# Kernel tuning notes

Hardware: AMD Instinct MI355X
Metric: run time of the kernel (lower is better)

The kernel has to match this reference:

```python
import jax, jax.numpy as jnp
import numpy as np

B, F, K = 8192, 4096, 64


def setup_inputs() -> dict:
    key = jax.random.key(0)
    kx, kv = jax.random.split(key)
    x = jax.random.normal(kx, (B, F), dtype=jnp.float32)
    # original init: uniform(-0.01, 0.01)
    v = jax.random.uniform(kv, (F, K), dtype=jnp.float32, minval=-0.01, maxval=0.01)
    return {"x": x, "v": v}


def reference(x, v):
    # sum_{i<j} <v_i, v_j> x_i x_j  ==  0.5 * sum_f ((x@v)_f^2 - (x^2 @ v^2)_f)
    xv = x @ v                      # [B, K]
    x2v2 = (x * x) @ (v * v)        # [B, K]
    res = 0.5 * jnp.sum(xv * xv - x2v2, axis=-1, keepdims=True)  # [B, 1]
    return res
```

## Files before the change

kernel.cpp:

```cpp
#include <hip/hip_runtime.h>
#include <hip/hip_bf16.h>


#define F_DIM 4096
#define K_DIM 64
#define B_ROWS 8192

typedef __attribute__((ext_vector_type(8))) short short8;
typedef __attribute__((ext_vector_type(4))) float float4v;
typedef __attribute__((ext_vector_type(16))) float f32x16;

__device__ __forceinline__ short f2bs(float f) {
    __hip_bfloat16 h = __float2bfloat16(f);
    short s;
    __builtin_memcpy(&s, &h, 2);
    return s;
}

__global__ void prep_kernel(const float* __restrict__ v,
                            short* __restrict__ vtf,
                            float* __restrict__ w) {
    __shared__ short lds_t[4][64][16];

    const int wid  = threadIdx.x >> 6;
    const int lane = threadIdx.x & 63;
    const int fc   = blockIdx.x * 4 + wid;
    const int r    = lane >> 2;
    const int k0   = (lane & 3) * 16;

    const float* src = v + (size_t)(fc * 16 + r) * K_DIM + k0;
    float vals[16];
#pragma unroll
    for (int i = 0; i < 16; i += 4) {
        float4v t = *(const float4v*)(src + i);
        vals[i] = t.x; vals[i+1] = t.y; vals[i+2] = t.z; vals[i+3] = t.w;
    }

    float sq = 0.0f;
#pragma unroll
    for (int i = 0; i < 16; ++i) sq += vals[i] * vals[i];
    sq += __shfl_xor(sq, 1, 64);
    sq += __shfl_xor(sq, 2, 64);
    if ((lane & 3) == 0) w[fc * 16 + r] = sq;

#pragma unroll
    for (int kk = 0; kk < 16; ++kk) lds_t[wid][k0 + kk][r] = f2bs(vals[kk]);
    __syncthreads();

#pragma unroll
    for (int c = 0; c < 2; ++c) {
        const short8 frag = *(const short8*)&lds_t[wid][c * 32 + (lane & 31)][8 * (lane >> 5)];
        *(short8*)(vtf + ((size_t)fc * 2 + c) * 512 + lane * 8) = frag;
    }
}

__launch_bounds__(1024, 4)
__global__ void fm_main_kernel(const float* __restrict__ x,
                               const short* __restrict__ vtf,
                               const float* __restrict__ w,
                               float* __restrict__ out) {
    __shared__ float yred[8][32][64];
    __shared__ float s1s[32];
    __shared__ float s2s[32];

    const int tid  = threadIdx.x;
    const int lane = tid & 63;
    const int wid  = tid >> 6;
    const int lrow = lane & 31;
    const int lk8  = (lane >> 5) * 8;
    const int row0 = blockIdx.x * 32;

    if (tid < 32) s2s[tid] = 0.0f;
    __syncthreads();

    const float* xrow = x + (size_t)(row0 + lrow) * F_DIM;
    const int fbase = wid * (F_DIM / 16);
    const int fcbase = fbase >> 4;

    f32x16 acc0{};
    f32x16 acc1{};
    float s2p = 0.0f;

#pragma unroll 2
    for (int ks = 0; ks < 16; ++ks) {
        const int fo = fbase + ks * 16 + lk8;
        const float4v xa = *(const float4v*)(xrow + fo);
        const float4v xb = *(const float4v*)(xrow + fo + 4);
        const float4v wa = *(const float4v*)(w + fo);
        const float4v wb = *(const float4v*)(w + fo + 4);

        s2p += xa.x*xa.x*wa.x + xa.y*xa.y*wa.y + xa.z*xa.z*wa.z + xa.w*xa.w*wa.w
             + xb.x*xb.x*wb.x + xb.y*xb.y*wb.y + xb.z*xb.z*wb.z + xb.w*xb.w*wb.w;

        short8 af;
        af[0]=f2bs(xa.x); af[1]=f2bs(xa.y); af[2]=f2bs(xa.z); af[3]=f2bs(xa.w);
        af[4]=f2bs(xb.x); af[5]=f2bs(xb.y); af[6]=f2bs(xb.z); af[7]=f2bs(xb.w);

        const size_t fc = (size_t)(fcbase + ks) * 2;
        const short8 b0 = *(const short8*)(vtf + (fc + 0) * 512 + lane * 8);
        const short8 b1 = *(const short8*)(vtf + (fc + 1) * 512 + lane * 8);

        acc0 = __builtin_amdgcn_mfma_f32_32x32x16_bf16(af, b0, acc0, 0, 0, 0);
        acc1 = __builtin_amdgcn_mfma_f32_32x32x16_bf16(af, b1, acc1, 0, 0, 0);
    }

    s2p += __shfl_xor(s2p, 32, 64);
    if (lane < 32) atomicAdd(&s2s[lrow], s2p);

    const int rbase = 4 * (lane >> 5);
    if (wid < 8) {
#pragma unroll
        for (int r = 0; r < 16; ++r) {
            const int row = (r & 3) + 8 * (r >> 2) + rbase;
            yred[wid][row][lrow]      = acc0[r];
            yred[wid][row][32 + lrow] = acc1[r];
        }
    }
    __syncthreads();
    if (wid >= 8) {
#pragma unroll
        for (int r = 0; r < 16; ++r) {
            const int row = (r & 3) + 8 * (r >> 2) + rbase;
            yred[wid - 8][row][lrow]      += acc0[r];
            yred[wid - 8][row][32 + lrow] += acc1[r];
        }
    }
    __syncthreads();

#pragma unroll
    for (int h = 0; h < 2; ++h) {
        const int row = 2 * wid + h;
        float y = 0.0f;
#pragma unroll
        for (int s = 0; s < 8; ++s) y += yred[s][row][lane];
        float yy = y * y;
#pragma unroll
        for (int m = 32; m >= 1; m >>= 1) yy += __shfl_xor(yy, m, 64);
        if (lane == 0) s1s[row] = yy;
    }
    __syncthreads();

    if (tid < 32) out[row0 + tid] = 0.5f * (s1s[tid] - s2s[tid]);
}

extern "C" void kernel_launch(void* const* d_in, const int* in_sizes, int n_in,
                              void* d_out, int out_size, void* d_ws, size_t ws_size,
                              hipStream_t stream) {
    const float* x = (const float*)d_in[0];
    const float* v = (const float*)d_in[1];
    float* out = (float*)d_out;

    short* vtf = (short*)d_ws;
    float* w = (float*)((char*)d_ws + (size_t)K_DIM * F_DIM * 2);

    prep_kernel<<<F_DIM / 16 / 4, 256, 0, stream>>>(v, vtf, w);
    fm_main_kernel<<<B_ROWS / 32, 1024, 0, stream>>>(x, vtf, w, out);
}
```

Before: 203.3 us.

## Stream x and V fragments through per-wave LDS ring via async global_load_lds

```diff
diff --git a/kernel.cpp b/kernel.cpp
--- a/kernel.cpp
+++ b/kernel.cpp
@@ -1,5 +1,6 @@
 #include <hip/hip_runtime.h>
 #include <hip/hip_bf16.h>
+#include <stdint.h>
 
 
 #define F_DIM 4096
@@ -9,6 +10,15 @@
 typedef __attribute__((ext_vector_type(8))) short short8;
 typedef __attribute__((ext_vector_type(4))) float float4v;
 typedef __attribute__((ext_vector_type(16))) float f32x16;
+
+typedef __attribute__((address_space(3))) uint32_t lds_u32;
+typedef const __attribute__((address_space(1))) uint32_t glb_u32;
+
+__device__ __forceinline__ void load_lds16(const void* g, void* l) {
+    __builtin_amdgcn_global_load_lds((glb_u32*)(uintptr_t)g,
+                                     (lds_u32*)(uint32_t)(uintptr_t)l,
+                                     16, 0, 0);
+}
 
 __device__ __forceinline__ short f2bs(float f) {
     __hip_bfloat16 h = __float2bfloat16(f);
@@ -54,40 +64,65 @@
     }
 }
 
-__launch_bounds__(1024, 4)
+__launch_bounds__(512, 2)
 __global__ void fm_main_kernel(const float* __restrict__ x,
                                const short* __restrict__ vtf,
                                const float* __restrict__ w,
                                float* __restrict__ out) {
-    __shared__ float yred[8][32][64];
-    __shared__ float s1s[32];
-    __shared__ float s2s[32];
+    __shared__ __align__(16) char ring[8][4][4096];
+    __shared__ __align__(16) float wlds[8][512];
+    __shared__ float s2red[8][32];
 
     const int tid  = threadIdx.x;
     const int lane = tid & 63;
     const int wid  = tid >> 6;
     const int lrow = lane & 31;
-    const int lk8  = (lane >> 5) * 8;
+    const int hi   = lane >> 5;
     const int row0 = blockIdx.x * 32;
+    const int fbase = wid * 512;
+    const int fcb2  = wid * 32;
 
-    if (tid < 32) s2s[tid] = 0.0f;
-    __syncthreads();
+    const float* gx_base = x + (size_t)(row0 + lrow) * F_DIM + fbase + hi * 4;
 
-    const float* xrow = x + (size_t)(row0 + lrow) * F_DIM;
-    const int fbase = wid * (F_DIM / 16);
-    const int fcbase = fbase >> 4;
+#define STAGE(t) do {                                                     \
+        char* eb_ = &ring[wid][(t) & 3][0];                               \
+        const float* gx_ = gx_base + (t) * 16;                            \
+        load_lds16(gx_,     eb_);                                         \
+        load_lds16(gx_ + 8, eb_ + 1024);                                  \
+        const short* gv_ = vtf + ((size_t)(fcb2 + (t))) * 1024 + lane * 8;\
+        load_lds16(gv_,       eb_ + 2048);                                \
+        load_lds16(gv_ + 512, eb_ + 3072);                                \
+    } while (0)
+
+    load_lds16(w + fbase + lane * 4,       &wlds[wid][0]);
+    load_lds16(w + fbase + 256 + lane * 4, &wlds[wid][256]);
+
+    STAGE(0); STAGE(1); STAGE(2);
 
     f32x16 acc0{};
     f32x16 acc1{};
     float s2p = 0.0f;
 
-#pragma unroll 2
-    for (int ks = 0; ks < 16; ++ks) {
-        const int fo = fbase + ks * 16 + lk8;
-        const float4v xa = *(const float4v*)(xrow + fo);
-        const float4v xb = *(const float4v*)(xrow + fo + 4);
-        const float4v wa = *(const float4v*)(w + fo);
-        const float4v wb = *(const float4v*)(w + fo + 4);
+    const int xoff = hi * 1024 + lrow * 16;
+    const int woff = hi * 32;
+
+#pragma unroll
+    for (int t = 0; t < 32; ++t) {
+        if (t + 3 < 32) STAGE(t + 3);
+        if (t < 29)       asm volatile("s_waitcnt vmcnt(12)" ::: "memory");
+        else if (t == 29) asm volatile("s_waitcnt vmcnt(8)"  ::: "memory");
+        else if (t == 30) asm volatile("s_waitcnt vmcnt(4)"  ::: "memory");
+        else              asm volatile("s_waitcnt vmcnt(0)"  ::: "memory");
+        __builtin_amdgcn_sched_barrier(0);
+
+        const char* eb = &ring[wid][t & 3][0];
+        const float4v xa = *(const float4v*)(eb + xoff);
+        const float4v xb = *(const float4v*)(eb + xoff + 512);
+        const short8  b0 = *(const short8*)(eb + 2048 + lane * 16);
+        const short8  b1 = *(const short8*)(eb + 3072 + lane * 16);
+        const char* wp = (const char*)&wlds[wid][0] + t * 64 + woff;
+        const float4v wa = *(const float4v*)(wp);
+        const float4v wb = *(const float4v*)(wp + 16);
 
         s2p += xa.x*xa.x*wa.x + xa.y*xa.y*wa.y + xa.z*xa.z*wa.z + xa.w*xa.w*wa.w
              + xb.x*xb.x*wb.x + xb.y*xb.y*wb.y + xb.z*xb.z*wb.z + xb.w*xb.w*wb.w;
@@ -96,51 +131,42 @@
         af[0]=f2bs(xa.x); af[1]=f2bs(xa.y); af[2]=f2bs(xa.z); af[3]=f2bs(xa.w);
         af[4]=f2bs(xb.x); af[5]=f2bs(xb.y); af[6]=f2bs(xb.z); af[7]=f2bs(xb.w);
 
-        const size_t fc = (size_t)(fcbase + ks) * 2;
-        const short8 b0 = *(const short8*)(vtf + (fc + 0) * 512 + lane * 8);
-        const short8 b1 = *(const short8*)(vtf + (fc + 1) * 512 + lane * 8);
-
         acc0 = __builtin_amdgcn_mfma_f32_32x32x16_bf16(af, b0, acc0, 0, 0, 0);
         acc1 = __builtin_amdgcn_mfma_f32_32x32x16_bf16(af, b1, acc1, 0, 0, 0);
     }
+#undef STAGE
 
     s2p += __shfl_xor(s2p, 32, 64);
-    if (lane < 32) atomicAdd(&s2s[lrow], s2p);
+    if (lane < 32) s2red[wid][lrow] = s2p;
 
-    const int rbase = 4 * (lane >> 5);
-    if (wid < 8) {
+    __syncthreads();
+
+    float (*yred)[32][64] = (float (*)[32][64])&ring[0][0][0];
+    const int rbase = 4 * hi;
 #pragma unroll
-        for (int r = 0; r < 16; ++r) {
-            const int row = (r & 3) + 8 * (r >> 2) + rbase;
-            yred[wid][row][lrow]      = acc0[r];
-            yred[wid][row][32 + lrow] = acc1[r];
-        }
-    }
-    __syncthreads();
-    if (wid >= 8) {
-#pragma unroll
-        for (int r = 0; r < 16; ++r) {
-            const int row = (r & 3) + 8 * (r >> 2) + rbase;
-            yred[wid - 8][row][lrow]      += acc0[r];
-            yred[wid - 8][row][32 + lrow] += acc1[r];
-        }
+    for (int r = 0; r < 16; ++r) {
+        const int row = (r & 3) + 8 * (r >> 2) + rbase;
+        yred[wid][row][lrow]      = acc0[r];
+        yred[wid][row][32 + lrow] = acc1[r];
     }
     __syncthreads();
 
 #pragma unroll
-    for (int h = 0; h < 2; ++h) {
-        const int row = 2 * wid + h;
+    for (int h = 0; h < 4; ++h) {
+        const int row = wid * 4 + h;
         float y = 0.0f;
 #pragma unroll
         for (int s = 0; s < 8; ++s) y += yred[s][row][lane];
         float yy = y * y;
 #pragma unroll
         for (int m = 32; m >= 1; m >>= 1) yy += __shfl_xor(yy, m, 64);
-        if (lane == 0) s1s[row] = yy;
+        if (lane == 0) {
+            float s2 = 0.0f;
+#pragma unroll
+            for (int s = 0; s < 8; ++s) s2 += s2red[s][row];
+            out[row0 + row] = 0.5f * (yy - s2);
+        }
     }
-    __syncthreads();
-
-    if (tid < 32) out[row0 + tid] = 0.5f * (s1s[tid] - s2s[tid]);
 }
 
 extern "C" void kernel_launch(void* const* d_in, const int* in_sizes, int n_in,
@@ -154,5 +180,5 @@
     float* w = (float*)((char*)d_ws + (size_t)K_DIM * F_DIM * 2);
 
     prep_kernel<<<F_DIM / 16 / 4, 256, 0, stream>>>(v, vtf, w);
-    fm_main_kernel<<<B_ROWS / 32, 1024, 0, stream>>>(x, vtf, w, out);
+    fm_main_kernel<<<B_ROWS / 32, 512, 0, stream>>>(x, vtf, w, out);
 }
```

Measured after the change: 199.9 us. About the same (-1.7%).
